# Kernel optimization log

Measured on AMD Instinct MI355X. Metric: run time of the kernel, lower is better.

## Reference

```python
import jax, jax.numpy as jnp
import numpy as np

H = 2  # num_heads hardcoded in the torch module


def setup_inputs() -> dict:
    key = jax.random.key(0)
    ks = jax.random.split(key, 10)
    B, S, D = 8, 2048, 512
    s = 0.02
    return {
        "rgb": jax.random.normal(ks[0], (B, S, D), jnp.float32),
        "event": jax.random.normal(ks[1], (B, S, D), jnp.float32),
        "w_rgb": jax.random.normal(ks[2], (D, D), jnp.float32) * s,
        "b_rgb": jnp.zeros((D,), jnp.float32),
        "w_event": jax.random.normal(ks[3], (D, D), jnp.float32) * s,
        "b_event": jnp.zeros((D,), jnp.float32),
        "w_in": jax.random.normal(ks[4], (3 * D, D), jnp.float32) * s,   # packed QKV in_proj, torch layout
        "b_in": jnp.zeros((3 * D,), jnp.float32),
        "w_out": jax.random.normal(ks[5], (D, D), jnp.float32) * s,
        "b_out": jnp.zeros((D,), jnp.float32),
    }


def _mha(q_in, kv_in, w_in, b_in, w_out, b_out):
    """torch nn.MultiheadAttention with key==value==kv_in, batch-first math."""
    B, S, D = q_in.shape
    hd = D // H
    q = q_in @ w_in[:D].T + b_in[:D]
    k = kv_in @ w_in[D:2 * D].T + b_in[D:2 * D]
    v = kv_in @ w_in[2 * D:].T + b_in[2 * D:]
    q = q.reshape(B, S, H, hd) * (1.0 / np.sqrt(hd))
    k = k.reshape(B, S, H, hd)
    v = v.reshape(B, S, H, hd)
    scores = jnp.einsum('bqhd,bkhd->bhqk', q, k)          # [B,H,S,S]
    attn = jax.nn.softmax(scores, axis=-1)
    out = jnp.einsum('bhqk,bkhd->bqhd', attn, v).reshape(B, S, D)
    return out @ w_out.T + b_out


def reference(rgb, event, w_rgb, b_rgb, w_event, b_event, w_in, b_in, w_out, b_out):
    rgb_p = rgb @ w_rgb.T + b_rgb
    event_p = event @ w_event.T + b_event
    # same attention weights used for both cross directions
    event_attn = _mha(rgb_p, event_p, w_in, b_in, w_out, b_out)
    rgb_attn = _mha(event_p, rgb_p, w_in, b_in, w_out, b_out)
    gate = jax.nn.sigmoid(jnp.sum(rgb_p * event_p, axis=-1, keepdims=True))
    fused = gate * event_attn + (1.0 - gate) * rgb_attn
    return fused + (rgb_p + event_p) * 0.5
```

## Files before the change

### kernel.cpp

```cpp
#include <hip/hip_runtime.h>
#include <hip/hip_bf16.h>
#include <stdint.h>


typedef __bf16 bf16_t;
typedef __bf16 bf16x8 __attribute__((ext_vector_type(8)));
typedef float f32x4 __attribute__((ext_vector_type(4)));
typedef float f32x16 __attribute__((ext_vector_type(16)));
typedef unsigned int u32;
typedef unsigned char u8;

typedef void gvoid_t __attribute__((address_space(1)));
typedef void svoid_t __attribute__((address_space(3)));

__device__ inline void gload16(const void* g, void* l) {
    __builtin_amdgcn_global_load_lds((gvoid_t*)g, (svoid_t*)l, 16, 0, 0);
}

__device__ inline float exp2v(float x) {
    float r;
    asm("v_exp_f32 %0, %1" : "=v"(r) : "v"(x));
    return r;
}

template <bool HI>
__device__ inline u32 pk_fp8(float a, float b, u32 old) {
    return (u32)__builtin_amdgcn_cvt_pk_fp8_f32(a, b, (int)old, HI);
}
__device__ inline u8 to_fp8(float a) { return (u8)(pk_fp8<false>(a, a, 0) & 0xff); }
__device__ inline long pk64(u32 lo, u32 hi) {
    return (long)(((unsigned long long)hi << 32) | (unsigned long long)lo);
}
__device__ inline f32x16 mfma_fp8(long a, long b, f32x16 c) {
    return __builtin_amdgcn_mfma_f32_32x32x16_fp8_fp8(a, b, c, 0, 0, 0);
}

__global__ __launch_bounds__(256) void f2b_w(const float* __restrict__ s2, bf16_t* __restrict__ d2,
                                             const float* __restrict__ s3, bf16_t* __restrict__ d3,
                                             const float* __restrict__ s4, bf16_t* __restrict__ d4,
                                             const float* __restrict__ s5, bf16_t* __restrict__ d5) {
    int i = blockIdx.x * 256 + threadIdx.x;
    const float* s; bf16_t* d; int off;
    if (i < 32768)       { s = s2; d = d2; off = i; }
    else if (i < 65536)  { s = s3; d = d3; off = i - 32768; }
    else if (i < 163840) { s = s4; d = d4; off = i - 65536; }
    else                 { s = s5; d = d5; off = i - 163840; }
    const float4* p = reinterpret_cast<const float4*>(s) + (size_t)off * 2;
    float4 a = p[0], b = p[1];
    bf16x8 o;
    o[0] = (bf16_t)a.x; o[1] = (bf16_t)a.y; o[2] = (bf16_t)a.z; o[3] = (bf16_t)a.w;
    o[4] = (bf16_t)b.x; o[5] = (bf16_t)b.y; o[6] = (bf16_t)b.z; o[7] = (bf16_t)b.w;
    reinterpret_cast<bf16x8*>(d)[off] = o;
}

template <int MODE>
__global__ __launch_bounds__(256) void gemm_bt(const float* __restrict__ Af,
                                               const float* __restrict__ Af2,
                                               const bf16_t* __restrict__ A,
                                               const bf16_t* __restrict__ A2,
                                               const bf16_t* __restrict__ Bw,
                                               const bf16_t* __restrict__ Bw2,
                                               const float* __restrict__ bias,
                                               const float* __restrict__ bias2,
                                               void* __restrict__ Cout,
                                               void* __restrict__ Cout2,
                                               const bf16_t* __restrict__ r1,
                                               const bf16_t* __restrict__ r2,
                                               const float* __restrict__ gate,
                                               u8* __restrict__ qdst,
                                               u8* __restrict__ kdst,
                                               u8* __restrict__ vdst,
                                               u8* __restrict__ qdst2,
                                               u8* __restrict__ kdst2,
                                               u8* __restrict__ vdst2,
                                               int N, int K) {
    __shared__ __align__(16) bf16_t As[128][64];
    __shared__ __align__(16) bf16_t Bs[128][64];
    const int tid = threadIdx.x, lane = tid & 63, w = tid >> 6;
    const int l16 = lane & 15, l4 = lane >> 4;
    const int wm = w >> 1, wn = w & 1;
    int xt, yt;
    if (MODE == 1) {
        int bid = blockIdx.x;
        int xcd = bid & 7, idx = bid >> 3;
        yt = xcd + 8 * (idx / 12);
        xt = idx % 12;
    } else {
        xt = blockIdx.x; yt = blockIdx.y;
    }
    const bool sec = (MODE != 2) && (yt >= 128);
    const size_t a0 = (size_t)(yt & 127) * 128;
    const size_t b0 = (size_t)xt * 128;
    const bf16_t* Ap = sec ? A2 : A;
    const bf16_t* Bp = sec ? Bw2 : Bw;
    const float* Afp = sec ? Af2 : Af;
    const float* bp = sec ? bias2 : bias;
    f32x4 acc[4][4] = {};
    const int srow = w * 32 + (lane >> 3);
    const int scol = (lane & 7) * 8;
    float g4[4];
    if (MODE == 2) {
#pragma unroll
        for (int i = 0; i < 4; ++i) g4[i] = gate[a0 + srow + i * 8];
    }
    for (int kt = 0; kt < K; kt += 64) {
        __syncthreads();
        if (MODE == 0) {
#pragma unroll
            for (int i = 0; i < 4; ++i) {
                const float4* p = reinterpret_cast<const float4*>(
                    Afp + (a0 + srow + i * 8) * (size_t)K + kt + scol);
                float4 x = p[0], y = p[1];
                bf16x8 o;
                o[0] = (bf16_t)x.x; o[1] = (bf16_t)x.y; o[2] = (bf16_t)x.z; o[3] = (bf16_t)x.w;
                o[4] = (bf16_t)y.x; o[5] = (bf16_t)y.y; o[6] = (bf16_t)y.z; o[7] = (bf16_t)y.w;
                *reinterpret_cast<bf16x8*>(&As[srow + i * 8][scol]) = o;
            }
        } else if (MODE == 2) {
#pragma unroll
            for (int i = 0; i < 4; ++i) {
                size_t ro = (a0 + srow + i * 8) * (size_t)K + kt + scol;
                bf16x8 x = *reinterpret_cast<const bf16x8*>(A + ro);
                bf16x8 y = *reinterpret_cast<const bf16x8*>(A2 + ro);
                bf16x8 o;
#pragma unroll
                for (int j = 0; j < 8; ++j)
                    o[j] = (bf16_t)(g4[i] * (float)x[j] + (1.f - g4[i]) * (float)y[j]);
                *reinterpret_cast<bf16x8*>(&As[srow + i * 8][scol]) = o;
            }
        } else {
#pragma unroll
            for (int i = 0; i < 4; ++i)
                gload16(Ap + (a0 + srow + i * 8) * (size_t)K + kt + scol, &As[w * 32 + i * 8][0]);
        }
#pragma unroll
        for (int i = 0; i < 4; ++i)
            gload16(Bp + (b0 + srow + i * 8) * (size_t)K + kt + scol, &Bs[w * 32 + i * 8][0]);
        __syncthreads();
#pragma unroll
        for (int kk = 0; kk < 2; ++kk) {
            bf16x8 af[4], bfr[4];
#pragma unroll
            for (int mi = 0; mi < 4; ++mi)
                af[mi] = *reinterpret_cast<const bf16x8*>(&As[wm * 64 + mi * 16 + l16][kk * 32 + l4 * 8]);
#pragma unroll
            for (int ni = 0; ni < 4; ++ni)
                bfr[ni] = *reinterpret_cast<const bf16x8*>(&Bs[wn * 64 + ni * 16 + l16][kk * 32 + l4 * 8]);
#pragma unroll
            for (int mi = 0; mi < 4; ++mi)
#pragma unroll
                for (int ni = 0; ni < 4; ++ni)
                    acc[mi][ni] = __builtin_amdgcn_mfma_f32_16x16x32_bf16(af[mi], bfr[ni], acc[mi][ni], 0, 0, 0);
        }
    }
    u8* qd = sec ? qdst2 : qdst;
    u8* kd = sec ? kdst2 : kdst;
    u8* vd = sec ? vdst2 : vdst;
#pragma unroll
    for (int mi = 0; mi < 4; ++mi) {
#pragma unroll
        for (int ni = 0; ni < 4; ++ni) {
            int col = (int)b0 + wn * 64 + ni * 16 + l16;
            float bs = bp[col];
            int row0 = (int)a0 + wm * 64 + mi * 16 + l4 * 4;
            float vv[4];
#pragma unroll
            for (int r = 0; r < 4; ++r) vv[r] = acc[mi][ni][r] + bs;
            if (MODE == 0) {
                bf16_t* Cp = (bf16_t*)(sec ? Cout2 : Cout);
#pragma unroll
                for (int r = 0; r < 4; ++r)
                    Cp[(size_t)(row0 + r) * N + col] = (bf16_t)vv[r];
            } else if (MODE == 2) {
#pragma unroll
                for (int r = 0; r < 4; ++r) {
                    size_t idx = (size_t)(row0 + r) * N + col;
                    ((float*)Cout)[idx] = vv[r] + 0.5f * ((float)r1[idx] + (float)r2[idx]);
                }
            } else {
                if (col < 512) {
#pragma unroll
                    for (int r = 0; r < 4; ++r)
                        qd[(size_t)(row0 + r) * 512 + col] = to_fp8(vv[r]);
                } else if (col < 1024) {
                    int cc = col - 512, hh = cc >> 8, d = cc & 255;
                    int dpart = ((d >> 3) & 1) * 128 + (d >> 4) * 8 + (d & 7);
#pragma unroll
                    for (int r = 0; r < 4; ++r) {
                        int row = row0 + r;
                        int bh = (row >> 11) * 2 + hh, seq = row & 2047;
                        int rr = seq & 31;
                        u32 boff = (u32)(rr * 256 + dpart) ^ (u32)((rr & 7) << 4);
                        kd[((size_t)(bh * 64 + (seq >> 5))) * 8192 + boff] = to_fp8(vv[r]);
                    }
                } else {
                    int cc = col - 1024, hh = cc >> 8, d = cc & 255;
                    int bh = (row0 >> 11) * 2 + hh, seq = row0 & 2047;
                    int k = seq & 31;
                    int s = (k >> 4) & 1, hik = (k >> 3) & 1, j0 = k & 7;
                    u32 wrd = pk_fp8<false>(vv[0], vv[1], 0);
                    wrd = pk_fp8<true>(vv[2], vv[3], wrd);
                    *reinterpret_cast<u32*>(vd + ((size_t)(bh * 64 + (seq >> 5))) * 8192 +
                                            d * 32 + hik * 16 + s * 8 + j0) = wrd;
                }
            }
        }
    }
}

__global__ __launch_bounds__(256) void gate_kernel(const bf16_t* __restrict__ rp,
                                                   const bf16_t* __restrict__ ep,
                                                   float* __restrict__ gate) {
    int row = blockIdx.x * 4 + (threadIdx.x >> 6);
    int lane = threadIdx.x & 63;
    bf16x8 a = reinterpret_cast<const bf16x8*>(rp + (size_t)row * 512)[lane];
    bf16x8 b = reinterpret_cast<const bf16x8*>(ep + (size_t)row * 512)[lane];
    float s = 0.f;
#pragma unroll
    for (int j = 0; j < 8; ++j) s += (float)a[j] * (float)b[j];
#pragma unroll
    for (int off = 32; off; off >>= 1) s += __shfl_xor(s, off, 64);
    if (lane == 0) gate[row] = 1.f / (1.f + __expf(-s));
}

__global__ __launch_bounds__(256, 2) void attn_kernel(const u8* __restrict__ qbr,
                                                      const u8* __restrict__ qbe,
                                                      const u8* __restrict__ kbr,
                                                      const u8* __restrict__ kbe,
                                                      const u8* __restrict__ vbr,
                                                      const u8* __restrict__ vbe,
                                                      bf16_t* __restrict__ out0,
                                                      bf16_t* __restrict__ out1) {
    __shared__ __align__(16) u8 smem[32768];
    const int bid = blockIdx.x;
    const int qb = bid >> 5;
    const int combo = bid & 31;
    const int dir = combo >> 4;
    const int bh = combo & 15;
    const int b = bh >> 1, h = bh & 1;
    const u8* Qb = dir ? qbe : qbr;
    const u8* Kc = dir ? kbr : kbe;
    const u8* Vc = dir ? vbr : vbe;
    bf16_t* osrc = dir ? out1 : out0;
    const int tid = threadIdx.x;
    const int w = tid >> 6, l = tid & 63;
    const int l31 = l & 31, hi = l >> 5;
    const int q0w = qb * 128 + w * 32;

    const u8* qp = Qb + ((size_t)(b * 2048 + q0w + l31)) * 512 + h * 256 + hi * 8;
    uint2 qf[16];
#pragma unroll
    for (int dch = 0; dch < 16; ++dch)
        qf[dch] = *reinterpret_cast<const uint2*>(qp + dch * 16);

    f32x16 O[8] = {};
    float mrun = -1e30f, lrun = 0.f;

    const u8* kq = Kc + (size_t)bh * 524288 + w * 2048 + l * 16;
    const u8* vq = Vc + (size_t)bh * 524288 + w * 2048 + l * 16;

#define STAGE(T, P)                                                          \
    do {                                                                     \
        const u8* ks_ = kq + (size_t)(T) * 8192;                             \
        const u8* vs_ = vq + (size_t)(T) * 8192;                             \
        gload16(ks_, &smem[(P) * 16384 + w * 2048]);                         \
        gload16(ks_ + 1024, &smem[(P) * 16384 + w * 2048 + 1024]);           \
        gload16(vs_, &smem[(P) * 16384 + 8192 + w * 2048]);                  \
        gload16(vs_ + 1024, &smem[(P) * 16384 + 8192 + w * 2048 + 1024]);    \
    } while (0)

    STAGE(0, 0);

    const u32 kx = (u32)((l31 & 7) << 4);
    for (int kt2 = 0; kt2 < 64; ++kt2) {
        asm volatile("s_waitcnt vmcnt(0)" ::: "memory");
        __builtin_amdgcn_s_barrier();
        if (kt2 < 63) STAGE(kt2 + 1, (kt2 + 1) & 1);

        const int cb = kt2 & 1;
        const u8* kbp = &smem[cb * 16384] + l31 * 256 + hi * 128;
        const u8* vg = &smem[cb * 16384 + 8192] + l31 * 32 + hi * 16;

        f32x16 st = {};
        __builtin_amdgcn_s_setprio(1);
#pragma unroll
        for (int m = 0; m < 8; ++m) {
            uint4 kk = *reinterpret_cast<const uint4*>(kbp + (((u32)(m << 4)) ^ kx));
            st = mfma_fp8(pk64(kk.x, kk.y), pk64(qf[2 * m].x, qf[2 * m].y), st);
            st = mfma_fp8(pk64(kk.z, kk.w), pk64(qf[2 * m + 1].x, qf[2 * m + 1].y), st);
        }
        __builtin_amdgcn_s_setprio(0);

#pragma unroll
        for (int r = 0; r < 16; ++r) st[r] *= 0.090168440f;

        float mx = st[0];
#pragma unroll
        for (int r = 1; r < 16; ++r) mx = fmaxf(mx, st[r]);
        mx = fmaxf(mx, __shfl_xor(mx, 32, 64));
        if (__any(mx - mrun > 8.f)) {
            float mnew = fmaxf(mrun, mx);
            float sc = exp2v(mrun - mnew);
            mrun = mnew;
            lrun *= sc;
#pragma unroll
            for (int r = 0; r < 16; ++r) {
                int qr = (r & 3) + 8 * (r >> 2) + 4 * hi;
                float scr = __shfl(sc, qr, 64);
#pragma unroll
                for (int g = 0; g < 8; ++g) O[g][r] *= scr;
            }
        }
        float p_[16];
        float lsum = 0.f;
#pragma unroll
        for (int r = 0; r < 16; ++r) { p_[r] = exp2v(st[r] - mrun); lsum += p_[r]; }
        lsum += __shfl_xor(lsum, 32, 64);
        lrun += lsum;

        u32 X0 = pk_fp8<false>(p_[0], p_[1], 0);   X0 = pk_fp8<true>(p_[2], p_[3], X0);
        u32 X1 = pk_fp8<false>(p_[4], p_[5], 0);   X1 = pk_fp8<true>(p_[6], p_[7], X1);
        u32 X2 = pk_fp8<false>(p_[8], p_[9], 0);   X2 = pk_fp8<true>(p_[10], p_[11], X2);
        u32 X3 = pk_fp8<false>(p_[12], p_[13], 0); X3 = pk_fp8<true>(p_[14], p_[15], X3);
        u32 E0 = (u32)__shfl_xor((int)(hi ? X0 : X1), 32, 64);
        u32 E1 = (u32)__shfl_xor((int)(hi ? X2 : X3), 32, 64);
        long A0 = pk64(hi ? E0 : X0, hi ? X1 : E0);
        long A1 = pk64(hi ? E1 : X2, hi ? X3 : E1);

        __builtin_amdgcn_s_setprio(1);
#pragma unroll
        for (int g = 0; g < 8; ++g) {
            uint4 v4 = *reinterpret_cast<const uint4*>(vg + g * 1024);
            O[g] = mfma_fp8(A0, pk64(v4.x, v4.y), O[g]);
            O[g] = mfma_fp8(A1, pk64(v4.z, v4.w), O[g]);
        }
        __builtin_amdgcn_s_setprio(0);
    }
#undef STAGE

#pragma unroll
    for (int r = 0; r < 16; ++r) {
        int qr = (r & 3) + 8 * (r >> 2) + 4 * hi;
        float linv = 1.0f / __shfl(lrun, qr, 64);
        size_t rowoff = ((size_t)(b * 2048 + q0w + qr)) * 512 + h * 256 + l31;
#pragma unroll
        for (int g = 0; g < 8; ++g)
            osrc[rowoff + g * 32] = (bf16_t)(O[g][r] * linv);
    }
}

extern "C" void kernel_launch(void* const* d_in, const int* in_sizes, int n_in,
                              void* d_out, int out_size, void* d_ws, size_t ws_size,
                              hipStream_t stream) {
    const float* rgb = (const float*)d_in[0];
    const float* event = (const float*)d_in[1];
    const float* w_rgb = (const float*)d_in[2];
    const float* b_rgb = (const float*)d_in[3];
    const float* w_event = (const float*)d_in[4];
    const float* b_event = (const float*)d_in[5];
    const float* w_in = (const float*)d_in[6];
    const float* b_in = (const float*)d_in[7];
    const float* w_out = (const float*)d_in[8];
    const float* b_out = (const float*)d_in[9];
    float* out = (float*)d_out;

    const size_t MB16 = (size_t)16 * 1024 * 1024;
    char* ws = (char*)d_ws;
    bf16_t* wrgb_bf = (bf16_t*)(ws + 0);
    bf16_t* wevt_bf = (bf16_t*)(ws + 524288);
    bf16_t* wout_bf = (bf16_t*)(ws + 1048576);
    bf16_t* win_bf = (bf16_t*)(ws + 1572864);
    float* gate = (float*)(ws + 3145728);
    bf16_t* bufA = (bf16_t*)(ws + 4194304);
    bf16_t* bufB = (bf16_t*)(ws + 4194304 + MB16);
    bf16_t* rgbp = (bf16_t*)(ws + 4194304 + 2 * MB16);
    bf16_t* evtp = (bf16_t*)(ws + 4194304 + 3 * MB16);
    u8* qbr = (u8*)(ws + 4194304 + 4 * MB16);
    u8* qbe = (u8*)(ws + 4194304 + 5 * MB16);
    u8* kbr = (u8*)(ws + 4194304 + 6 * MB16);
    u8* kbe = (u8*)(ws + 4194304 + 7 * MB16);
    u8* vbr = (u8*)(ws + 4194304 + 8 * MB16);
    u8* vbe = (u8*)(ws + 4194304 + 9 * MB16);

    dim3 blk(256);
    f2b_w<<<768, blk, 0, stream>>>(w_rgb, wrgb_bf, w_event, wevt_bf,
                                   w_in, win_bf, w_out, wout_bf);
    gemm_bt<0><<<dim3(4, 256), blk, 0, stream>>>(rgb, event, nullptr, nullptr,
                                                 wrgb_bf, wevt_bf, b_rgb, b_event,
                                                 rgbp, evtp, nullptr, nullptr, nullptr,
                                                 nullptr, nullptr, nullptr, nullptr, nullptr,
                                                 nullptr, 512, 512);
    gate_kernel<<<4096, blk, 0, stream>>>(rgbp, evtp, gate);
    gemm_bt<1><<<3072, blk, 0, stream>>>(nullptr, nullptr, rgbp, evtp, win_bf, win_bf,
                                         b_in, b_in, nullptr, nullptr, nullptr, nullptr,
                                         nullptr, qbr, kbr, vbr, qbe, kbe, vbe, 1536, 512);
    attn_kernel<<<512, blk, 0, stream>>>(qbr, qbe, kbr, kbe, vbr, vbe, bufA, bufB);
    gemm_bt<2><<<dim3(4, 128), blk, 0, stream>>>(nullptr, nullptr, bufA, bufB, wout_bf, nullptr,
                                                 b_out, nullptr, out, nullptr, rgbp, evtp, gate,
                                                 nullptr, nullptr, nullptr, nullptr, nullptr,
                                                 nullptr, 512, 512);
}
```

Before: 303.3 us.

## Process two K/V tiles per attention iteration and swizzle V in LDS

The attention loop now stages and consumes two 32-key K/V tiles per iteration (64 keys), halving the number of barriers, waits and softmax max/rescale passes. LDS per block doubles to 64KB. The V tile layout written by the projection kernel gains an XOR swizzle matching the reader to reduce LDS bank conflicts. This raises register and LDS pressure, which may limit occupancy at two blocks per CU.

```diff
diff --git a/kernel.cpp b/kernel.cpp
--- a/kernel.cpp
+++ b/kernel.cpp
@@ -200,8 +200,8 @@
                     int s = (k >> 4) & 1, hik = (k >> 3) & 1, j0 = k & 7;
                     u32 wrd = pk_fp8<false>(vv[0], vv[1], 0);
                     wrd = pk_fp8<true>(vv[2], vv[3], wrd);
-                    *reinterpret_cast<u32*>(vd + ((size_t)(bh * 64 + (seq >> 5))) * 8192 +
-                                            d * 32 + hik * 16 + s * 8 + j0) = wrd;
+                    u32 boff = (u32)(d * 32 + hik * 16 + s * 8 + j0) ^ (u32)((d & 7) << 4);
+                    *reinterpret_cast<u32*>(vd + ((size_t)(bh * 64 + (seq >> 5))) * 8192 + boff) = wrd;
                 }
             }
         }
@@ -231,7 +231,7 @@
                                                       const u8* __restrict__ vbe,
                                                       bf16_t* __restrict__ out0,
                                                       bf16_t* __restrict__ out1) {
-    __shared__ __align__(16) u8 smem[32768];
+    __shared__ __align__(16) u8 smem[65536];
     const int bid = blockIdx.x;
     const int qb = bid >> 5;
     const int combo = bid & 31;
@@ -256,47 +256,57 @@
     f32x16 O[8] = {};
     float mrun = -1e30f, lrun = 0.f;
 
-    const u8* kq = Kc + (size_t)bh * 524288 + w * 2048 + l * 16;
-    const u8* vq = Vc + (size_t)bh * 524288 + w * 2048 + l * 16;
+    const u8* kq = Kc + (size_t)bh * 524288 + w * 4096 + l * 16;
+    const u8* vq = Vc + (size_t)bh * 524288 + w * 4096 + l * 16;
 
 #define STAGE(T, P)                                                          \
     do {                                                                     \
-        const u8* ks_ = kq + (size_t)(T) * 8192;                             \
-        const u8* vs_ = vq + (size_t)(T) * 8192;                             \
-        gload16(ks_, &smem[(P) * 16384 + w * 2048]);                         \
-        gload16(ks_ + 1024, &smem[(P) * 16384 + w * 2048 + 1024]);           \
-        gload16(vs_, &smem[(P) * 16384 + 8192 + w * 2048]);                  \
-        gload16(vs_ + 1024, &smem[(P) * 16384 + 8192 + w * 2048 + 1024]);    \
+        const u8* ks_ = kq + (size_t)(T) * 16384;                            \
+        const u8* vs_ = vq + (size_t)(T) * 16384;                            \
+        gload16(ks_, &smem[(P) * 32768 + w * 4096]);                         \
+        gload16(ks_ + 1024, &smem[(P) * 32768 + w * 4096 + 1024]);           \
+        gload16(ks_ + 2048, &smem[(P) * 32768 + w * 4096 + 2048]);           \
+        gload16(ks_ + 3072, &smem[(P) * 32768 + w * 4096 + 3072]);           \
+        gload16(vs_, &smem[(P) * 32768 + 16384 + w * 4096]);                 \
+        gload16(vs_ + 1024, &smem[(P) * 32768 + 16384 + w * 4096 + 1024]);   \
+        gload16(vs_ + 2048, &smem[(P) * 32768 + 16384 + w * 4096 + 2048]);   \
+        gload16(vs_ + 3072, &smem[(P) * 32768 + 16384 + w * 4096 + 3072]);   \
     } while (0)
 
     STAGE(0, 0);
 
     const u32 kx = (u32)((l31 & 7) << 4);
-    for (int kt2 = 0; kt2 < 64; ++kt2) {
+    for (int kt2 = 0; kt2 < 32; ++kt2) {
         asm volatile("s_waitcnt vmcnt(0)" ::: "memory");
         __builtin_amdgcn_s_barrier();
-        if (kt2 < 63) STAGE(kt2 + 1, (kt2 + 1) & 1);
+        if (kt2 < 31) STAGE(kt2 + 1, (kt2 + 1) & 1);
 
         const int cb = kt2 & 1;
-        const u8* kbp = &smem[cb * 16384] + l31 * 256 + hi * 128;
-        const u8* vg = &smem[cb * 16384 + 8192] + l31 * 32 + hi * 16;
-
-        f32x16 st = {};
+        const u8* kb0 = &smem[cb * 32768] + l31 * 256 + hi * 128;
+        const u8* vg = &smem[cb * 32768 + 16384] + (((u32)(l31 * 32 + hi * 16)) ^ kx);
+
+        f32x16 st0 = {}, st1 = {};
         __builtin_amdgcn_s_setprio(1);
 #pragma unroll
         for (int m = 0; m < 8; ++m) {
-            uint4 kk = *reinterpret_cast<const uint4*>(kbp + (((u32)(m << 4)) ^ kx));
-            st = mfma_fp8(pk64(kk.x, kk.y), pk64(qf[2 * m].x, qf[2 * m].y), st);
-            st = mfma_fp8(pk64(kk.z, kk.w), pk64(qf[2 * m + 1].x, qf[2 * m + 1].y), st);
+            uint4 ka = *reinterpret_cast<const uint4*>(kb0 + (((u32)(m << 4)) ^ kx));
+            st0 = mfma_fp8(pk64(ka.x, ka.y), pk64(qf[2 * m].x, qf[2 * m].y), st0);
+            st0 = mfma_fp8(pk64(ka.z, ka.w), pk64(qf[2 * m + 1].x, qf[2 * m + 1].y), st0);
+            uint4 kc = *reinterpret_cast<const uint4*>(kb0 + 8192 + (((u32)(m << 4)) ^ kx));
+            st1 = mfma_fp8(pk64(kc.x, kc.y), pk64(qf[2 * m].x, qf[2 * m].y), st1);
+            st1 = mfma_fp8(pk64(kc.z, kc.w), pk64(qf[2 * m + 1].x, qf[2 * m + 1].y), st1);
         }
         __builtin_amdgcn_s_setprio(0);
 
 #pragma unroll
-        for (int r = 0; r < 16; ++r) st[r] *= 0.090168440f;
-
-        float mx = st[0];
-#pragma unroll
-        for (int r = 1; r < 16; ++r) mx = fmaxf(mx, st[r]);
+        for (int r = 0; r < 16; ++r) {
+            st0[r] *= 0.090168440f;
+            st1[r] *= 0.090168440f;
+        }
+
+        float mx = fmaxf(st0[0], st1[0]);
+#pragma unroll
+        for (int r = 1; r < 16; ++r) mx = fmaxf(mx, fmaxf(st0[r], st1[r]));
         mx = fmaxf(mx, __shfl_xor(mx, 32, 64));
         if (__any(mx - mrun > 8.f)) {
             float mnew = fmaxf(mrun, mx);
@@ -311,21 +321,32 @@
                 for (int g = 0; g < 8; ++g) O[g][r] *= scr;
             }
         }
-        float p_[16];
         float lsum = 0.f;
 #pragma unroll
-        for (int r = 0; r < 16; ++r) { p_[r] = exp2v(st[r] - mrun); lsum += p_[r]; }
+        for (int r = 0; r < 16; ++r) {
+            st0[r] = exp2v(st0[r] - mrun);
+            st1[r] = exp2v(st1[r] - mrun);
+            lsum += st0[r] + st1[r];
+        }
         lsum += __shfl_xor(lsum, 32, 64);
         lrun += lsum;
 
-        u32 X0 = pk_fp8<false>(p_[0], p_[1], 0);   X0 = pk_fp8<true>(p_[2], p_[3], X0);
-        u32 X1 = pk_fp8<false>(p_[4], p_[5], 0);   X1 = pk_fp8<true>(p_[6], p_[7], X1);
-        u32 X2 = pk_fp8<false>(p_[8], p_[9], 0);   X2 = pk_fp8<true>(p_[10], p_[11], X2);
-        u32 X3 = pk_fp8<false>(p_[12], p_[13], 0); X3 = pk_fp8<true>(p_[14], p_[15], X3);
+        u32 X0 = pk_fp8<false>(st0[0], st0[1], 0);    X0 = pk_fp8<true>(st0[2], st0[3], X0);
+        u32 X1 = pk_fp8<false>(st0[4], st0[5], 0);    X1 = pk_fp8<true>(st0[6], st0[7], X1);
+        u32 X2 = pk_fp8<false>(st0[8], st0[9], 0);    X2 = pk_fp8<true>(st0[10], st0[11], X2);
+        u32 X3 = pk_fp8<false>(st0[12], st0[13], 0);  X3 = pk_fp8<true>(st0[14], st0[15], X3);
+        u32 X4 = pk_fp8<false>(st1[0], st1[1], 0);    X4 = pk_fp8<true>(st1[2], st1[3], X4);
+        u32 X5 = pk_fp8<false>(st1[4], st1[5], 0);    X5 = pk_fp8<true>(st1[6], st1[7], X5);
+        u32 X6 = pk_fp8<false>(st1[8], st1[9], 0);    X6 = pk_fp8<true>(st1[10], st1[11], X6);
+        u32 X7 = pk_fp8<false>(st1[12], st1[13], 0);  X7 = pk_fp8<true>(st1[14], st1[15], X7);
         u32 E0 = (u32)__shfl_xor((int)(hi ? X0 : X1), 32, 64);
         u32 E1 = (u32)__shfl_xor((int)(hi ? X2 : X3), 32, 64);
+        u32 E2 = (u32)__shfl_xor((int)(hi ? X4 : X5), 32, 64);
+        u32 E3 = (u32)__shfl_xor((int)(hi ? X6 : X7), 32, 64);
         long A0 = pk64(hi ? E0 : X0, hi ? X1 : E0);
         long A1 = pk64(hi ? E1 : X2, hi ? X3 : E1);
+        long A2 = pk64(hi ? E2 : X4, hi ? X5 : E2);
+        long A3 = pk64(hi ? E3 : X6, hi ? X7 : E3);
 
         __builtin_amdgcn_s_setprio(1);
 #pragma unroll
@@ -333,6 +354,9 @@
             uint4 v4 = *reinterpret_cast<const uint4*>(vg + g * 1024);
             O[g] = mfma_fp8(A0, pk64(v4.x, v4.y), O[g]);
             O[g] = mfma_fp8(A1, pk64(v4.z, v4.w), O[g]);
+            uint4 v5 = *reinterpret_cast<const uint4*>(vg + 8192 + g * 1024);
+            O[g] = mfma_fp8(A2, pk64(v5.x, v5.y), O[g]);
+            O[g] = mfma_fp8(A3, pk64(v5.z, v5.w), O[g]);
         }
         __builtin_amdgcn_s_setprio(0);
     }
```

New measurement: 314.3 us. 1.04x slower.
